# Kernel tuning notes

Measured on AMD Instinct MI355X. Metric: run time of the kernel, lower is better.

The kernel has to match this reference:

```python
import jax, jax.numpy as jnp
import numpy as np

B, C, L, H = 4, 512, 2048, 8
D = C // H  # head_dim


def setup_inputs() -> dict:
    key = jax.random.key(0)
    ks = jax.random.split(key, 9)
    s = 1.0 / np.sqrt(C)  # keep logits well-scaled like torch Linear init
    return {
        "x": jax.random.normal(ks[0], (B, C, L), dtype=jnp.float32),
        "Wq": jax.random.normal(ks[1], (C, C), dtype=jnp.float32) * s,
        "bq": jnp.zeros((C,), dtype=jnp.float32),
        "Wk": jax.random.normal(ks[2], (C, C), dtype=jnp.float32) * s,
        "bk": jnp.zeros((C,), dtype=jnp.float32),
        "Wv": jax.random.normal(ks[3], (C, C), dtype=jnp.float32) * s,
        "bv": jnp.zeros((C,), dtype=jnp.float32),
        "Wo": jax.random.normal(ks[4], (C, C), dtype=jnp.float32) * s,
        "bo": jnp.zeros((C,), dtype=jnp.float32),
    }


def reference(x, Wq, bq, Wk, bk, Wv, bv, Wo, bo):
    # x: (B, C, L) -> (B, L, C)
    xp = jnp.transpose(x, (0, 2, 1))
    scale = D ** (-0.5)

    def heads(w, b):
        y = xp @ w.T + b                      # (B, L, C)  torch Linear: x W^T + b
        return y.reshape(B, L, H, D).transpose(0, 2, 1, 3)  # (B, H, L, D)

    q = heads(Wq, bq)
    k = heads(Wk, bk)
    v = heads(Wv, bv)

    attn = jnp.einsum('bhqd,bhkd->bhqk', q, k) * scale  # (B, H, L, L)
    attn = jax.nn.softmax(attn, axis=-1)
    out = jnp.einsum('bhqk,bhkd->bhqd', attn, v)        # (B, H, L, D)
    out = out.transpose(0, 2, 1, 3).reshape(B, L, C)    # (B, L, C)
    out = out @ Wo.T + bo
    return x + jnp.transpose(out, (0, 2, 1))            # residual in (B, C, L)
```

## Files before the change

### kernel.cpp

```cpp
#include <hip/hip_runtime.h>
#include <math.h>

#define B_ 4
#define C_ 512
#define L_ 2048
#define H_ 8
#define D_ 64
#define QSCALE 0.18033688011112042f
#define DEFER_THR 12.0f

typedef __bf16 bf16x8 __attribute__((ext_vector_type(8)));
typedef float f32x4 __attribute__((ext_vector_type(4)));
typedef float f32x16 __attribute__((ext_vector_type(16)));

__device__ __forceinline__ unsigned cvt_pk(float lo, float hi) {
    unsigned r;
    asm("v_cvt_pk_bf16_f32 %0, %1, %2" : "=v"(r) : "v"(lo), "v"(hi));
    return r;
}
__device__ __forceinline__ unsigned short f2bf_hw(float a) {
    unsigned r;
    asm("v_cvt_pk_bf16_f32 %0, %1, %1" : "=v"(r) : "v"(a));
    return (unsigned short)r;
}
__device__ __forceinline__ bf16x8 frag_ld(const unsigned short* p) {
    uint4 v = *reinterpret_cast<const uint4*>(p);
    return __builtin_bit_cast(bf16x8, v);
}
__device__ __forceinline__ float fmax3(float a, float b, float c) {
    return fmaxf(fmaxf(a, b), c);
}
__device__ __forceinline__ void glds16(const void* g, void* l) {
    __builtin_amdgcn_global_load_lds(
        (const __attribute__((address_space(1))) void*)g,
        (__attribute__((address_space(3))) void*)l, 16, 0, 0);
}

__global__ __launch_bounds__(256) void prep(
    const float* __restrict__ x,
    const float* __restrict__ w0, const float* __restrict__ w1,
    const float* __restrict__ w2, const float* __restrict__ w3,
    unsigned short* __restrict__ xt,
    unsigned short* __restrict__ o0, unsigned short* __restrict__ o1,
    unsigned short* __restrict__ o2, unsigned short* __restrict__ o3)
{
    __shared__ float T[64][68];
    const int t = threadIdx.x;

    if (blockIdx.z < B_) {
        const int b  = blockIdx.z;
        const int l0 = blockIdx.x * 64;
        const int c0 = blockIdx.y * 64;
        const float* xb = x + (size_t)b * C_ * L_;
        unsigned short* xtb = xt + (size_t)b * L_ * C_;

        #pragma unroll
        for (int p = 0; p < 4; ++p) {
            const int ci = 16 * p + (t >> 4);
            const int l4 = (t & 15) * 4;
            *reinterpret_cast<float4*>(&T[ci][l4]) =
                *reinterpret_cast<const float4*>(xb + (size_t)(c0 + ci) * L_ + l0 + l4);
        }
        __syncthreads();

        const int lo = t >> 2;
        const int cb = (t & 3) * 16;
        unsigned w[8];
        #pragma unroll
        for (int k = 0; k < 8; ++k)
            w[k] = cvt_pk(T[cb + 2 * k][lo], T[cb + 2 * k + 1][lo]);
        unsigned short* dst = xtb + (size_t)(l0 + lo) * C_ + c0 + cb;
        *reinterpret_cast<uint4*>(dst)     = make_uint4(w[0], w[1], w[2], w[3]);
        *reinterpret_cast<uint4*>(dst + 8) = make_uint4(w[4], w[5], w[6], w[7]);
    } else {
        const int m = blockIdx.z - B_;
        const float* src; unsigned short* dst;
        if      (m == 0) { src = w0; dst = o0; }
        else if (m == 1) { src = w1; dst = o1; }
        else if (m == 2) { src = w2; dst = o2; }
        else             { src = w3; dst = o3; }
        const int flat = blockIdx.x + 32 * blockIdx.y;
        const size_t idx = ((size_t)flat * 256 + t) * 4;
        const float4 v = *reinterpret_cast<const float4*>(src + idx);
        *reinterpret_cast<uint2*>(dst + idx) =
            make_uint2(cvt_pk(v.x, v.y), cvt_pk(v.z, v.w));
    }
}

__global__ __launch_bounds__(256) void qkv_gemm(
    const unsigned short* __restrict__ xt,
    const unsigned short* __restrict__ wq, const unsigned short* __restrict__ wk,
    const unsigned short* __restrict__ wv,
    const float* __restrict__ bq, const float* __restrict__ bk,
    const float* __restrict__ bv,
    unsigned short* __restrict__ qb, unsigned short* __restrict__ kb,
    unsigned short* __restrict__ vb)
{
    __shared__ unsigned short As[2][128][32];
    __shared__ unsigned short Bs[2][128][32];

    const int mode = blockIdx.z >> 2;
    const int b    = blockIdx.z & 3;
    const size_t LC = (size_t)L_ * C_;

    const unsigned short *A, *Bt;
    const float* bias;
    unsigned short* Out;
    float scale = 1.0f;
    int m0, n0, oN, biasN;
    if (mode == 0) {
        A = xt + (size_t)b * LC; Bt = wq; bias = bq; Out = qb + (size_t)b * LC;
        m0 = blockIdx.y * 128; n0 = blockIdx.x * 128; oN = C_; biasN = 1;
        scale = QSCALE;
    } else if (mode == 1) {
        A = xt + (size_t)b * LC; Bt = wk; bias = bk; Out = kb + (size_t)b * LC;
        m0 = blockIdx.y * 128; n0 = blockIdx.x * 128; oN = C_; biasN = 1;
    } else {
        A = wv; Bt = xt + (size_t)b * LC; bias = bv; Out = vb + (size_t)b * LC;
        m0 = blockIdx.x * 128; n0 = blockIdx.y * 128; oN = L_; biasN = 0;
    }
    const int doswz = (mode != 0);

    const int t = threadIdx.x;
    const int lane = t & 63, wid = t >> 6;
    const int wm = (wid >> 1) * 64, wn = (wid & 1) * 64;
    const int q16 = lane & 15, g = lane >> 4;

    const int gr = wid * 32 + (lane >> 2);
    const int gc = (lane & 3) * 8;
    const unsigned short* Ap0 = A  + (size_t)(m0 + gr) * C_ + gc;
    const unsigned short* Ap1 = Ap0 + 16 * C_;
    const unsigned short* Bp0 = Bt + (size_t)(n0 + gr) * C_ + gc;
    const unsigned short* Bp1 = Bp0 + 16 * C_;

    f32x4 zero4 = {0.f, 0.f, 0.f, 0.f};
    f32x4 acc[4][4];
    #pragma unroll
    for (int i = 0; i < 4; ++i)
        #pragma unroll
        for (int j = 0; j < 4; ++j) acc[i][j] = zero4;

    glds16(Ap0, &As[0][wid * 32][0]);      glds16(Ap1, &As[0][wid * 32 + 16][0]);
    glds16(Bp0, &Bs[0][wid * 32][0]);      glds16(Bp1, &Bs[0][wid * 32 + 16][0]);
    __syncthreads();

    #pragma unroll 2
    for (int it = 0; it < 16; ++it) {
        const int cur = it & 1;
        if (it < 15) {
            const int ko = (it + 1) * 32;
            glds16(Ap0 + ko, &As[cur ^ 1][wid * 32][0]);
            glds16(Ap1 + ko, &As[cur ^ 1][wid * 32 + 16][0]);
            glds16(Bp0 + ko, &Bs[cur ^ 1][wid * 32][0]);
            glds16(Bp1 + ko, &Bs[cur ^ 1][wid * 32 + 16][0]);
        }
        bf16x8 af[4], bfr[4];
        #pragma unroll
        for (int i = 0; i < 4; ++i) af[i]  = frag_ld(&As[cur][wm + 16 * i + q16][8 * g]);
        #pragma unroll
        for (int j = 0; j < 4; ++j) bfr[j] = frag_ld(&Bs[cur][wn + 16 * j + q16][8 * g]);
        #pragma unroll
        for (int i = 0; i < 4; ++i)
            #pragma unroll
            for (int j = 0; j < 4; ++j)
                acc[i][j] = __builtin_amdgcn_mfma_f32_16x16x32_bf16(
                    af[i], bfr[j], acc[i][j], 0, 0, 0);
        __syncthreads();
    }

    #pragma unroll
    for (int j = 0; j < 4; ++j) {
        const int n = n0 + wn + 16 * j + q16;
        const float bn = biasN ? bias[n] : 0.f;
        #pragma unroll
        for (int i = 0; i < 4; ++i) {
            #pragma unroll
            for (int r = 0; r < 4; ++r) {
                const int m = m0 + wm + 16 * i + 4 * g + r;
                const float v = acc[i][j][r] + (biasN ? bn : bias[m]);
                const int nn = doswz ? (n ^ ((m & 7) << 3)) : n;
                Out[(size_t)m * oN + nn] = f2bf_hw(v * scale);
            }
        }
    }
}

__global__ __launch_bounds__(256) void gemm_out(
    const unsigned short* __restrict__ A,
    const unsigned short* __restrict__ Bt,
    const float* __restrict__ bias,
    float* __restrict__ Out, const float* __restrict__ resid)
{
    __shared__ unsigned short As[2][128][32];
    __shared__ unsigned short Bs[2][128][32];

    const int bz = blockIdx.z;
    const size_t LC = (size_t)L_ * C_;
    Bt    += (size_t)bz * LC;
    Out   += (size_t)bz * LC;
    resid += (size_t)bz * LC;

    const int n0 = blockIdx.x * 128;
    const int m0 = blockIdx.y * 128;
    const int t  = threadIdx.x;
    const int lane = t & 63, wid = t >> 6;
    const int wm = (wid >> 1) * 64, wn = (wid & 1) * 64;
    const int q16 = lane & 15, g = lane >> 4;

    const int gr = wid * 32 + (lane >> 2);
    const int gc = (lane & 3) * 8;
    const unsigned short* Ap0 = A  + (size_t)(m0 + gr) * C_ + gc;
    const unsigned short* Ap1 = Ap0 + 16 * C_;
    const unsigned short* Bp0 = Bt + (size_t)(n0 + gr) * C_ + gc;
    const unsigned short* Bp1 = Bp0 + 16 * C_;

    f32x4 zero4 = {0.f, 0.f, 0.f, 0.f};
    f32x4 acc[4][4];
    #pragma unroll
    for (int i = 0; i < 4; ++i)
        #pragma unroll
        for (int j = 0; j < 4; ++j) acc[i][j] = zero4;

    glds16(Ap0, &As[0][wid * 32][0]);      glds16(Ap1, &As[0][wid * 32 + 16][0]);
    glds16(Bp0, &Bs[0][wid * 32][0]);      glds16(Bp1, &Bs[0][wid * 32 + 16][0]);
    __syncthreads();

    #pragma unroll 2
    for (int it = 0; it < 16; ++it) {
        const int cur = it & 1;
        if (it < 15) {
            const int ko = (it + 1) * 32;
            glds16(Ap0 + ko, &As[cur ^ 1][wid * 32][0]);
            glds16(Ap1 + ko, &As[cur ^ 1][wid * 32 + 16][0]);
            glds16(Bp0 + ko, &Bs[cur ^ 1][wid * 32][0]);
            glds16(Bp1 + ko, &Bs[cur ^ 1][wid * 32 + 16][0]);
        }
        bf16x8 af[4], bfr[4];
        #pragma unroll
        for (int i = 0; i < 4; ++i) af[i]  = frag_ld(&As[cur][wm + 16 * i + q16][8 * g]);
        #pragma unroll
        for (int j = 0; j < 4; ++j) bfr[j] = frag_ld(&Bs[cur][wn + 16 * j + q16][8 * g]);
        #pragma unroll
        for (int i = 0; i < 4; ++i)
            #pragma unroll
            for (int j = 0; j < 4; ++j)
                acc[i][j] = __builtin_amdgcn_mfma_f32_16x16x32_bf16(
                    af[i], bfr[j], acc[i][j], 0, 0, 0);
        __syncthreads();
    }

    #pragma unroll
    for (int j = 0; j < 4; ++j) {
        const int n = n0 + wn + 16 * j + q16;
        #pragma unroll
        for (int i = 0; i < 4; ++i) {
            #pragma unroll
            for (int r = 0; r < 4; ++r) {
                const int m = m0 + wm + 16 * i + 4 * g + r;
                const size_t off = (size_t)m * L_ + n;
                Out[off] = acc[i][j][r] + bias[m] + resid[off];
            }
        }
    }
}

__global__ __launch_bounds__(256) void attn_mfma(
    const unsigned short* __restrict__ Qb,
    const unsigned short* __restrict__ Kb,
    const unsigned short* __restrict__ Vb,
    unsigned short* __restrict__ Ab)
{
    __shared__ unsigned short Ks[2][64][64];
    __shared__ unsigned short Vs[2][64][64];

    const int q0 = blockIdx.x * 128;
    const int h  = blockIdx.y;
    const int b  = blockIdx.z;
    const int t  = threadIdx.x, lane = t & 63, wid = t >> 6;
    const int q32 = lane & 31, hi = lane >> 5;
    const int swz = (q32 & 7) << 3;

    const unsigned short* Qg = Qb + (size_t)b * L_ * C_;
    const unsigned short* Kg = Kb + (size_t)b * L_ * C_ + h * D_;
    const unsigned short* Vg = Vb + ((size_t)b * C_ + h * D_) * L_;
    unsigned short* Ag       = Ab + (size_t)b * L_ * C_;

    bf16x8 qf[4];
    {
        const unsigned short* qp =
            Qg + (size_t)(q0 + 32 * wid + q32) * C_ + h * D_ + 8 * hi;
        #pragma unroll
        for (int c = 0; c < 4; ++c) qf[c] = frag_ld(qp + 16 * c);
    }

    const unsigned ow = (q32 == 0) ? 0x3F803F80u : 0u;
    const uint4 ov = make_uint4(ow, ow, ow, ow);
    const bf16x8 onesf = __builtin_bit_cast(bf16x8, ov);

    f32x16 zero16 = {0.f,0.f,0.f,0.f,0.f,0.f,0.f,0.f,
                     0.f,0.f,0.f,0.f,0.f,0.f,0.f,0.f};
    f32x16 oacc0 = zero16, oacc1 = zero16, lacc = zero16;
    float m_s = -INFINITY;

    const int gr8 = lane >> 3;
    const int gc8 = (lane & 7) * 8;
    const unsigned short* Kp0 = Kg + (size_t)(16 * wid + gr8) * C_ + gc8;
    const unsigned short* Kp1 = Kp0 + (size_t)8 * C_;
    const unsigned short* Vp0 = Vg + (size_t)(16 * wid + gr8) * L_ + gc8;
    const unsigned short* Vp1 = Vp0 + (size_t)8 * L_;

    glds16(Kp0, &Ks[0][16 * wid][0]);
    glds16(Kp1, &Ks[0][16 * wid + 8][0]);
    glds16(Vp0, &Vs[0][16 * wid][0]);
    glds16(Vp1, &Vs[0][16 * wid + 8][0]);
    __syncthreads();

    #pragma unroll 2
    for (int kt = 0; kt < 32; ++kt) {
        const int cur = kt & 1;
        if (kt < 31) {
            const size_t ko = (size_t)(kt + 1) * 64;
            glds16(Kp0 + ko * C_, &Ks[cur ^ 1][16 * wid][0]);
            glds16(Kp1 + ko * C_, &Ks[cur ^ 1][16 * wid + 8][0]);
            glds16(Vp0 + ko,      &Vs[cur ^ 1][16 * wid][0]);
            glds16(Vp1 + ko,      &Vs[cur ^ 1][16 * wid + 8][0]);
        }

        f32x16 s0 = zero16, s1 = zero16;
        #pragma unroll
        for (int c = 0; c < 4; ++c) {
            const int co = (16 * c + 8 * hi) ^ swz;
            bf16x8 k0 = frag_ld(&Ks[cur][q32][co]);
            bf16x8 k1 = frag_ld(&Ks[cur][32 + q32][co]);
            s0 = __builtin_amdgcn_mfma_f32_32x32x16_bf16(k0, qf[c], s0, 0, 0, 0);
            s1 = __builtin_amdgcn_mfma_f32_32x32x16_bf16(k1, qf[c], s1, 0, 0, 0);
        }

        const float a0 = fmax3(s0[0], s0[1], s0[2]);
        const float a1 = fmax3(s0[3], s0[4], s0[5]);
        const float a2 = fmax3(s0[6], s0[7], s0[8]);
        const float a3 = fmax3(s0[9], s0[10], s0[11]);
        const float a4 = fmax3(s0[12], s0[13], s0[14]);
        const float a5 = fmax3(s0[15], s1[0], s1[1]);
        const float a6 = fmax3(s1[2], s1[3], s1[4]);
        const float a7 = fmax3(s1[5], s1[6], s1[7]);
        const float a8 = fmax3(s1[8], s1[9], s1[10]);
        const float a9 = fmax3(s1[11], s1[12], s1[13]);
        const float b0 = fmax3(a0, a1, a2);
        const float b1 = fmax3(a3, a4, a5);
        const float b2 = fmax3(a6, a7, a8);
        const float b3 = fmax3(a9, s1[14], s1[15]);
        float pm = fmaxf(fmaxf(b0, b1), fmaxf(b2, b3));
        pm = fmaxf(pm, __shfl_xor(pm, 32));

        if (!__all(pm - m_s <= DEFER_THR)) {
            const float mn   = fmaxf(m_s, pm);
            const float corr = exp2f(m_s - mn);
            m_s = mn;
            #pragma unroll
            for (int r = 0; r < 16; ++r) {
                const float cr = __shfl(corr, (r & 3) + 8 * (r >> 2) + 4 * hi);
                oacc0[r] *= cr; oacc1[r] *= cr; lacc[r] *= cr;
            }
        }

        float p0[16], p1[16];
        #pragma unroll
        for (int r = 0; r < 16; ++r) {
            p0[r] = exp2f(s0[r] - m_s);
            p1[r] = exp2f(s1[r] - m_s);
        }

        #pragma unroll
        for (int ks = 0; ks < 4; ++ks) {
            const int rb = 8 * (ks & 1);
            #define PPX(i) ((ks < 2) ? p0[(i)] : p1[(i)])
            unsigned wa = cvt_pk(PPX(rb + 0), PPX(rb + 1));
            unsigned wb = cvt_pk(PPX(rb + 2), PPX(rb + 3));
            unsigned wc = cvt_pk(PPX(rb + 4), PPX(rb + 5));
            unsigned wd = cvt_pk(PPX(rb + 6), PPX(rb + 7));
            #undef PPX
            asm volatile("v_permlane32_swap_b32 %0, %1" : "+v"(wa), "+v"(wc));
            asm volatile("v_permlane32_swap_b32 %0, %1" : "+v"(wb), "+v"(wd));
            const uint4 pv = make_uint4(wa, wb, wc, wd);
            const bf16x8 paf = __builtin_bit_cast(bf16x8, pv);

            const int co = (16 * ks + 8 * hi) ^ swz;
            bf16x8 v0 = frag_ld(&Vs[cur][q32][co]);
            bf16x8 v1 = frag_ld(&Vs[cur][32 + q32][co]);
            oacc0 = __builtin_amdgcn_mfma_f32_32x32x16_bf16(paf, v0, oacc0, 0, 0, 0);
            oacc1 = __builtin_amdgcn_mfma_f32_32x32x16_bf16(paf, v1, oacc1, 0, 0, 0);
            lacc  = __builtin_amdgcn_mfma_f32_32x32x16_bf16(paf, onesf, lacc, 0, 0, 0);
        }

        __syncthreads();
    }

    #pragma unroll
    for (int r = 0; r < 16; ++r) {
        const float lv  = __shfl(lacc[r], hi << 5);
        const float inv = 1.f / lv;
        const int q = q0 + 32 * wid + (r & 3) + 8 * (r >> 2) + 4 * hi;
        unsigned short* op = Ag + (size_t)q * C_ + h * D_ + q32;
        op[0]  = f2bf_hw(oacc0[r] * inv);
        op[32] = f2bf_hw(oacc1[r] * inv);
    }
}

extern "C" void kernel_launch(void* const* d_in, const int* in_sizes, int n_in,
                              void* d_out, int out_size, void* d_ws, size_t ws_size,
                              hipStream_t stream)
{
    const float* x  = (const float*)d_in[0];
    const float* Wq = (const float*)d_in[1];
    const float* bq = (const float*)d_in[2];
    const float* Wk = (const float*)d_in[3];
    const float* bk = (const float*)d_in[4];
    const float* Wv = (const float*)d_in[5];
    const float* bv = (const float*)d_in[6];
    const float* Wo = (const float*)d_in[7];
    const float* bo = (const float*)d_in[8];
    float* out = (float*)d_out;

    const size_t NB = (size_t)B_ * L_ * C_;
    const size_t NW = (size_t)C_ * C_;
    unsigned short* ws16 = (unsigned short*)d_ws;
    unsigned short* xt  = ws16;
    unsigned short* qb  = xt  + NB;
    unsigned short* kb  = qb  + NB;
    unsigned short* vb  = kb  + NB;
    unsigned short* att = vb  + NB;
    unsigned short* wqb = att + NB;
    unsigned short* wkb = wqb + NW;
    unsigned short* wvb = wkb + NW;
    unsigned short* wob = wvb + NW;

    prep<<<dim3(32, 8, 2 * B_), 256, 0, stream>>>(
        x, Wq, Wk, Wv, Wo, xt, wqb, wkb, wvb, wob);

    qkv_gemm<<<dim3(4, 16, 3 * B_), 256, 0, stream>>>(
        xt, wqb, wkb, wvb, bq, bk, bv, qb, kb, vb);

    attn_mfma<<<dim3(L_ / 128, H_, B_), 256, 0, stream>>>(qb, kb, vb, att);

    gemm_out<<<dim3(16, 4, B_), 256, 0, stream>>>(wob, att, bo, out, x);
}
```

Before: 208.6 us.

## Rework GEMM staging, pad transpose tile, add MFMA priority hints in attention

The prep transpose tile is padded to 65 columns and filled with scalar stores. qkv_gemm drops its double-buffered LDS prefetch for a single buffer with a sync before and after each load. gemm_out now uses register prefetch into a padded 40-column LDS tile. The attention kernel wraps its MFMA sections in s_setprio and vectorises the max subtraction before exp2. The single-buffer qkv path loses load/compute overlap, which may cancel the gains from the other changes.

```diff
diff --git a/kernel.cpp b/kernel.cpp
--- a/kernel.cpp
+++ b/kernel.cpp
@@ -44,7 +44,7 @@
     unsigned short* __restrict__ o0, unsigned short* __restrict__ o1,
     unsigned short* __restrict__ o2, unsigned short* __restrict__ o3)
 {
-    __shared__ float T[64][68];
+    __shared__ float T[64][65];
     const int t = threadIdx.x;
 
     if (blockIdx.z < B_) {
@@ -58,8 +58,10 @@
         for (int p = 0; p < 4; ++p) {
             const int ci = 16 * p + (t >> 4);
             const int l4 = (t & 15) * 4;
-            *reinterpret_cast<float4*>(&T[ci][l4]) =
-                *reinterpret_cast<const float4*>(xb + (size_t)(c0 + ci) * L_ + l0 + l4);
+            const float4 v = *reinterpret_cast<const float4*>(
+                xb + (size_t)(c0 + ci) * L_ + l0 + l4);
+            T[ci][l4 + 0] = v.x; T[ci][l4 + 1] = v.y;
+            T[ci][l4 + 2] = v.z; T[ci][l4 + 3] = v.w;
         }
         __syncthreads();
 
@@ -96,8 +98,8 @@
     unsigned short* __restrict__ qb, unsigned short* __restrict__ kb,
     unsigned short* __restrict__ vb)
 {
-    __shared__ unsigned short As[2][128][32];
-    __shared__ unsigned short Bs[2][128][32];
+    __shared__ unsigned short As[128][32];
+    __shared__ unsigned short Bs[128][32];
 
     const int mode = blockIdx.z >> 2;
     const int b    = blockIdx.z & 3;
@@ -132,6 +134,10 @@
     const unsigned short* Ap1 = Ap0 + 16 * C_;
     const unsigned short* Bp0 = Bt + (size_t)(n0 + gr) * C_ + gc;
     const unsigned short* Bp1 = Bp0 + 16 * C_;
+    unsigned short* lA0 = &As[wid * 32][0];
+    unsigned short* lA1 = &As[wid * 32 + 16][0];
+    unsigned short* lB0 = &Bs[wid * 32][0];
+    unsigned short* lB1 = &Bs[wid * 32 + 16][0];
 
     f32x4 zero4 = {0.f, 0.f, 0.f, 0.f};
     f32x4 acc[4][4];
@@ -140,32 +146,22 @@
         #pragma unroll
         for (int j = 0; j < 4; ++j) acc[i][j] = zero4;
 
-    glds16(Ap0, &As[0][wid * 32][0]);      glds16(Ap1, &As[0][wid * 32 + 16][0]);
-    glds16(Bp0, &Bs[0][wid * 32][0]);      glds16(Bp1, &Bs[0][wid * 32 + 16][0]);
-    __syncthreads();
-
-    #pragma unroll 2
-    for (int it = 0; it < 16; ++it) {
-        const int cur = it & 1;
-        if (it < 15) {
-            const int ko = (it + 1) * 32;
-            glds16(Ap0 + ko, &As[cur ^ 1][wid * 32][0]);
-            glds16(Ap1 + ko, &As[cur ^ 1][wid * 32 + 16][0]);
-            glds16(Bp0 + ko, &Bs[cur ^ 1][wid * 32][0]);
-            glds16(Bp1 + ko, &Bs[cur ^ 1][wid * 32 + 16][0]);
-        }
+    for (int k0 = 0; k0 < C_; k0 += 32) {
+        __syncthreads();
+        glds16(Ap0 + k0, lA0); glds16(Ap1 + k0, lA1);
+        glds16(Bp0 + k0, lB0); glds16(Bp1 + k0, lB1);
+        __syncthreads();
         bf16x8 af[4], bfr[4];
         #pragma unroll
-        for (int i = 0; i < 4; ++i) af[i]  = frag_ld(&As[cur][wm + 16 * i + q16][8 * g]);
-        #pragma unroll
-        for (int j = 0; j < 4; ++j) bfr[j] = frag_ld(&Bs[cur][wn + 16 * j + q16][8 * g]);
+        for (int i = 0; i < 4; ++i) af[i]  = frag_ld(&As[wm + 16 * i + q16][8 * g]);
+        #pragma unroll
+        for (int j = 0; j < 4; ++j) bfr[j] = frag_ld(&Bs[wn + 16 * j + q16][8 * g]);
         #pragma unroll
         for (int i = 0; i < 4; ++i)
             #pragma unroll
             for (int j = 0; j < 4; ++j)
                 acc[i][j] = __builtin_amdgcn_mfma_f32_16x16x32_bf16(
                     af[i], bfr[j], acc[i][j], 0, 0, 0);
-        __syncthreads();
     }
 
     #pragma unroll
@@ -191,8 +187,8 @@
     const float* __restrict__ bias,
     float* __restrict__ Out, const float* __restrict__ resid)
 {
-    __shared__ unsigned short As[2][128][32];
-    __shared__ unsigned short Bs[2][128][32];
+    __shared__ unsigned short As[128][40];
+    __shared__ unsigned short Bs[128][40];
 
     const int bz = blockIdx.z;
     const size_t LC = (size_t)L_ * C_;
@@ -207,12 +203,10 @@
     const int wm = (wid >> 1) * 64, wn = (wid & 1) * 64;
     const int q16 = lane & 15, g = lane >> 4;
 
-    const int gr = wid * 32 + (lane >> 2);
-    const int gc = (lane & 3) * 8;
-    const unsigned short* Ap0 = A  + (size_t)(m0 + gr) * C_ + gc;
-    const unsigned short* Ap1 = Ap0 + 16 * C_;
-    const unsigned short* Bp0 = Bt + (size_t)(n0 + gr) * C_ + gc;
-    const unsigned short* Bp1 = Bp0 + 16 * C_;
+    const int srow = t >> 1;
+    const int scol = (t & 1) * 16;
+    const unsigned short* Ap = A  + (size_t)(m0 + srow) * C_ + scol;
+    const unsigned short* Bp = Bt + (size_t)(n0 + srow) * C_ + scol;
 
     f32x4 zero4 = {0.f, 0.f, 0.f, 0.f};
     f32x4 acc[4][4];
@@ -221,32 +215,35 @@
         #pragma unroll
         for (int j = 0; j < 4; ++j) acc[i][j] = zero4;
 
-    glds16(Ap0, &As[0][wid * 32][0]);      glds16(Ap1, &As[0][wid * 32 + 16][0]);
-    glds16(Bp0, &Bs[0][wid * 32][0]);      glds16(Bp1, &Bs[0][wid * 32 + 16][0]);
-    __syncthreads();
-
-    #pragma unroll 2
-    for (int it = 0; it < 16; ++it) {
-        const int cur = it & 1;
-        if (it < 15) {
-            const int ko = (it + 1) * 32;
-            glds16(Ap0 + ko, &As[cur ^ 1][wid * 32][0]);
-            glds16(Ap1 + ko, &As[cur ^ 1][wid * 32 + 16][0]);
-            glds16(Bp0 + ko, &Bs[cur ^ 1][wid * 32][0]);
-            glds16(Bp1 + ko, &Bs[cur ^ 1][wid * 32 + 16][0]);
+    uint4 ar0 = *reinterpret_cast<const uint4*>(Ap);
+    uint4 ar1 = *reinterpret_cast<const uint4*>(Ap + 8);
+    uint4 br0 = *reinterpret_cast<const uint4*>(Bp);
+    uint4 br1 = *reinterpret_cast<const uint4*>(Bp + 8);
+
+    for (int k0 = 0; k0 < C_; k0 += 32) {
+        __syncthreads();
+        *reinterpret_cast<uint4*>(&As[srow][scol])     = ar0;
+        *reinterpret_cast<uint4*>(&As[srow][scol + 8]) = ar1;
+        *reinterpret_cast<uint4*>(&Bs[srow][scol])     = br0;
+        *reinterpret_cast<uint4*>(&Bs[srow][scol + 8]) = br1;
+        __syncthreads();
+        if (k0 + 32 < C_) {
+            ar0 = *reinterpret_cast<const uint4*>(Ap + k0 + 32);
+            ar1 = *reinterpret_cast<const uint4*>(Ap + k0 + 40);
+            br0 = *reinterpret_cast<const uint4*>(Bp + k0 + 32);
+            br1 = *reinterpret_cast<const uint4*>(Bp + k0 + 40);
         }
         bf16x8 af[4], bfr[4];
         #pragma unroll
-        for (int i = 0; i < 4; ++i) af[i]  = frag_ld(&As[cur][wm + 16 * i + q16][8 * g]);
-        #pragma unroll
-        for (int j = 0; j < 4; ++j) bfr[j] = frag_ld(&Bs[cur][wn + 16 * j + q16][8 * g]);
+        for (int i = 0; i < 4; ++i) af[i]  = frag_ld(&As[wm + 16 * i + q16][8 * g]);
+        #pragma unroll
+        for (int j = 0; j < 4; ++j) bfr[j] = frag_ld(&Bs[wn + 16 * j + q16][8 * g]);
         #pragma unroll
         for (int i = 0; i < 4; ++i)
             #pragma unroll
             for (int j = 0; j < 4; ++j)
                 acc[i][j] = __builtin_amdgcn_mfma_f32_16x16x32_bf16(
                     af[i], bfr[j], acc[i][j], 0, 0, 0);
-        __syncthreads();
     }
 
     #pragma unroll
@@ -327,6 +324,7 @@
         }
 
         f32x16 s0 = zero16, s1 = zero16;
+        __builtin_amdgcn_s_setprio(1);
         #pragma unroll
         for (int c = 0; c < 4; ++c) {
             const int co = (16 * c + 8 * hi) ^ swz;
@@ -335,6 +333,7 @@
             s0 = __builtin_amdgcn_mfma_f32_32x32x16_bf16(k0, qf[c], s0, 0, 0, 0);
             s1 = __builtin_amdgcn_mfma_f32_32x32x16_bf16(k1, qf[c], s1, 0, 0, 0);
         }
+        __builtin_amdgcn_s_setprio(0);
 
         const float a0 = fmax3(s0[0], s0[1], s0[2]);
         const float a1 = fmax3(s0[3], s0[4], s0[5]);
@@ -364,13 +363,19 @@
             }
         }
 
+        f32x16 ms16;
+        #pragma unroll
+        for (int r = 0; r < 16; ++r) ms16[r] = m_s;
+        const f32x16 d0 = s0 - ms16;
+        const f32x16 d1 = s1 - ms16;
         float p0[16], p1[16];
         #pragma unroll
         for (int r = 0; r < 16; ++r) {
-            p0[r] = exp2f(s0[r] - m_s);
-            p1[r] = exp2f(s1[r] - m_s);
-        }
-
+            p0[r] = exp2f(d0[r]);
+            p1[r] = exp2f(d1[r]);
+        }
+
+        __builtin_amdgcn_s_setprio(1);
         #pragma unroll
         for (int ks = 0; ks < 4; ++ks) {
             const int rb = 8 * (ks & 1);
@@ -392,6 +397,7 @@
             oacc1 = __builtin_amdgcn_mfma_f32_32x32x16_bf16(paf, v1, oacc1, 0, 0, 0);
             lacc  = __builtin_amdgcn_mfma_f32_32x32x16_bf16(paf, onesf, lacc, 0, 0, 0);
         }
+        __builtin_amdgcn_s_setprio(0);
 
         __syncthreads();
     }
```

After: 199.3 us. 4.4% less time.
